# Kernel optimization log

Hardware: AMD Instinct MI355X
Metric: run time of the kernel (lower is better)

## Reference

```python
import jax, jax.numpy as jnp
import numpy as np

N = 1536       # n_nodes
D_IN = 256     # in_features
D_OUT = 64     # out_features (= n_hidden, n_heads=1, is_concat=True)
N_WAY = 16     # known_attacks_count
SLOPE = 0.2    # LeakyReLU negative slope


def setup_inputs() -> dict:
    key = jax.random.key(0)
    k1, k2, k3, k4, k5 = jax.random.split(key, 5)
    hidden_vectors = jax.random.normal(k1, (N, D_IN), dtype=jnp.float32)
    labels = jax.random.randint(k2, (N, 1), 0, N_WAY)
    zda_mask = jax.random.randint(k3, (N, 1), 0, 2).astype(bool)
    # deterministic support/query split: first half support, last half query
    query_mask = jnp.concatenate([jnp.zeros(N // 2, bool), jnp.ones(N // 2, bool)])
    W = jax.random.normal(k4, (D_OUT, D_IN), jnp.float32) * (1.0 / np.sqrt(D_IN))
    attn_w = jax.random.normal(k5, (D_OUT,), jnp.float32) * (1.0 / np.sqrt(D_OUT))
    return {"hidden_vectors": hidden_vectors, "W": W, "attn_w": attn_w,
            "labels": labels, "zda_mask": zda_mask, "query_mask": query_mask,
            "known_attacks_count": N_WAY}


def _forward(hidden_vectors, W, attn_w, labels, zda_mask, n_way):
    n = hidden_vectors.shape[0]
    dt = hidden_vectors.dtype
    # one-hot labels (scatter equivalent)
    oh = jax.nn.one_hot(labels[:, 0], n_way, dtype=dt)                 # [n, n_way]
    known = ~zda_mask[:, 0]                                            # unknown == zda
    ohm = jnp.where(known[:, None], oh, jnp.zeros((), dt))             # masked one-hot
    # collaborative kernel: semantic similarity between known pairs, else 1
    sem = ohm @ ohm.T                                                  # [n, n]
    cond = known[:, None] & known[None, :]
    kernel = jnp.where(cond, sem, jnp.ones((), dt))
    # GATv2 with shared weights, 1 head: e[i,j] = attn . lrelu(g[i] + g[j])
    g = hidden_vectors @ W.T                                           # [n, d_out]
    s = g[:, None, :] + g[None, :, :]                                  # [n, n, d_out]
    s = jnp.where(s >= 0, s, SLOPE * s)                                # LeakyReLU
    e = jnp.einsum('ijd,d->ij', s, attn_w)                             # [n, n]
    e = jnp.where(kernel == 0.0, -jnp.inf, e)                          # colaborative mask
    a = jax.nn.softmax(e, axis=1)                                      # [n, n]
    h_out = a @ g                                                      # [n, d_out] (concat, 1 head)
    # centroids over support nodes (first half)
    n_sup = n // 2
    h_sup, oh_sup = h_out[:n_sup], oh[:n_sup]
    agg = oh_sup.T @ h_sup                                             # [n_way, d_out]
    counts = oh_sup.sum(0)                                             # [n_way]
    centroids = jnp.where((counts > 0)[:, None],
                          agg / jnp.maximum(counts, 1.0)[:, None], 0.0)
    # inverse euclidean distance scores for query nodes (last half)
    hq = h_out[n_sup:]
    d2 = (jnp.sum(hq * hq, 1)[:, None] + jnp.sum(centroids * centroids, 1)[None, :]
          - 2.0 * hq @ centroids.T)
    dist = jnp.sqrt(jnp.maximum(d2, 0.0))
    scores = 1.0 / (dist + 1e-10)
    return scores, h_out, a


def reference(hidden_vectors, W, attn_w, labels, zda_mask, query_mask, known_attacks_count):
    return _forward(hidden_vectors, W, attn_w, labels, zda_mask, known_attacks_count)
```

## Files before the change

kernel.cpp:

```cpp
#include <hip/hip_runtime.h>
#include <math.h>

#define NN 1536
#define DIN 256
#define DOUT 64
#define NWAY 16
#define NSUP 768
#define IB 12
#define JBLK 256
#define SROWS 3

#define OFF_SCORES 0
#define OFF_H 12288
#define OFF_A 110592

#define WG 0
#define WQ 98304
#define WCODE 99840
#define WCENT 101376

__global__ __launch_bounds__(256) void k_g(const float* __restrict__ hid,
                                           const float* __restrict__ W,
                                           const float* __restrict__ attw,
                                           const int* __restrict__ labels,
                                           const int* __restrict__ zda,
                                           float* __restrict__ g,
                                           float* __restrict__ q,
                                           int* __restrict__ code) {
  int t = threadIdx.x;
  int r = t >> 6, d = t & 63;
  int i = blockIdx.x * 4 + r;
  const float4* hp = (const float4*)(hid + (size_t)i * DIN);
  const float4* wp = (const float4*)(W + (size_t)d * DIN);
  float4 acc = {0.f, 0.f, 0.f, 0.f};
#pragma unroll
  for (int k = 0; k < DIN / 4; k++) {
    float4 h4 = hp[k];
    float4 w4 = wp[k];
    acc.x = fmaf(h4.x, w4.x, acc.x);
    acc.y = fmaf(h4.y, w4.y, acc.y);
    acc.z = fmaf(h4.z, w4.z, acc.z);
    acc.w = fmaf(h4.w, w4.w, acc.w);
  }
  float gv = (acc.x + acc.y) + (acc.z + acc.w);
  g[(size_t)i * DOUT + d] = gv;
  float val = gv * attw[d];
#pragma unroll
  for (int off = 32; off >= 1; off >>= 1) val += __shfl_xor(val, off, 64);
  if (d == 0) q[i] = 0.6f * val;
  if (t < 4) {
    int ii = blockIdx.x * 4 + t;
    code[ii] = zda[ii] ? -1 : labels[ii];
  }
}

__global__ __launch_bounds__(256, 2) void k_e(const float* __restrict__ g,
                                              const float* __restrict__ q,
                                              const int* __restrict__ code,
                                              const float* __restrict__ attw,
                                              float* __restrict__ aout) {
  __shared__ float gis[IB * DOUT];
  __shared__ float lp[4][IB][JBLK];
  __shared__ float qi[IB];
  __shared__ int ci[IB];
  int t = threadIdx.x;
  int lane = t & 63;
  int w = t >> 6;
  int wq = __builtin_amdgcn_readfirstlane(w);
  int i0 = blockIdx.x * IB;
  int j0 = blockIdx.y * JBLK;

  if (t < IB * 16) {
    ((float4*)gis)[t] = ((const float4*)(g + (size_t)i0 * DOUT))[t];
  } else if (t < IB * 16 + IB) {
    int u = t - IB * 16;
    qi[u] = q[i0 + u];
    ci[u] = code[i0 + u];
  }
  float4 gj0[4], gj1[4], gj2[4], gj3[4];
  {
    const float4* p0 = (const float4*)(g + (size_t)(j0 + lane) * DOUT + wq * 16);
    const float4* p1 = (const float4*)(g + (size_t)(j0 + 64 + lane) * DOUT + wq * 16);
    const float4* p2 = (const float4*)(g + (size_t)(j0 + 128 + lane) * DOUT + wq * 16);
    const float4* p3 = (const float4*)(g + (size_t)(j0 + 192 + lane) * DOUT + wq * 16);
#pragma unroll
    for (int k = 0; k < 4; k++) gj0[k] = p0[k];
#pragma unroll
    for (int k = 0; k < 4; k++) gj1[k] = p1[k];
#pragma unroll
    for (int k = 0; k < 4; k++) gj2[k] = p2[k];
#pragma unroll
    for (int k = 0; k < 4; k++) gj3[k] = p3[k];
  }
  const float4* wv = (const float4*)(attw + wq * 16);
  __syncthreads();

#pragma unroll 1
  for (int u = 0; u < IB; u++) {
    const float4* gv = (const float4*)(gis + u * DOUT + wq * 16);
    float4 a0 = {0,0,0,0}, a1 = {0,0,0,0}, a2 = {0,0,0,0}, a3 = {0,0,0,0};
#pragma unroll
    for (int k = 0; k < 4; k++) {
      float4 a4 = gv[k];
      float4 w4 = wv[k];
      float4 b;
      b = gj0[k];
      a0.x = fmaf(w4.x, fabsf(a4.x + b.x), a0.x);
      a0.y = fmaf(w4.y, fabsf(a4.y + b.y), a0.y);
      a0.z = fmaf(w4.z, fabsf(a4.z + b.z), a0.z);
      a0.w = fmaf(w4.w, fabsf(a4.w + b.w), a0.w);
      b = gj1[k];
      a1.x = fmaf(w4.x, fabsf(a4.x + b.x), a1.x);
      a1.y = fmaf(w4.y, fabsf(a4.y + b.y), a1.y);
      a1.z = fmaf(w4.z, fabsf(a4.z + b.z), a1.z);
      a1.w = fmaf(w4.w, fabsf(a4.w + b.w), a1.w);
      b = gj2[k];
      a2.x = fmaf(w4.x, fabsf(a4.x + b.x), a2.x);
      a2.y = fmaf(w4.y, fabsf(a4.y + b.y), a2.y);
      a2.z = fmaf(w4.z, fabsf(a4.z + b.z), a2.z);
      a2.w = fmaf(w4.w, fabsf(a4.w + b.w), a2.w);
      b = gj3[k];
      a3.x = fmaf(w4.x, fabsf(a4.x + b.x), a3.x);
      a3.y = fmaf(w4.y, fabsf(a4.y + b.y), a3.y);
      a3.z = fmaf(w4.z, fabsf(a4.z + b.z), a3.z);
      a3.w = fmaf(w4.w, fabsf(a4.w + b.w), a3.w);
    }
    lp[w][u][lane] = (a0.x + a0.y) + (a0.z + a0.w);
    lp[w][u][lane + 64] = (a1.x + a1.y) + (a1.z + a1.w);
    lp[w][u][lane + 128] = (a2.x + a2.y) + (a2.z + a2.w);
    lp[w][u][lane + 192] = (a3.x + a3.y) + (a3.z + a3.w);
  }
  __syncthreads();

  int jg = j0 + t;
  float qj = q[jg];
  int cj = code[jg];
#pragma unroll
  for (int u = 0; u < IB; u++) {
    float s = (lp[0][u][t] + lp[1][u][t]) + (lp[2][u][t] + lp[3][u][t]);
    float e = (qi[u] + qj) + 0.4f * s;
    int cu = ci[u];
    if ((cu >= 0) && (cj >= 0) && (cu != cj)) e = -1e30f;
    aout[(size_t)(i0 + u) * NN + jg] = e;
  }
}

__global__ __launch_bounds__(512) void k_smh(float* __restrict__ a,
                                             const float* __restrict__ g,
                                             float* __restrict__ h) {
  __shared__ float buf[32 * SROWS * 68];
  __shared__ float red[16];
  float* al = buf;
  int t = threadIdx.x;
  int lane = t & 63;
  int w = t >> 6;
  int r0 = blockIdx.x * SROWS;

#pragma unroll 1
  for (int r = 0; r < SROWS; r++) {
    float* row = a + (size_t)(r0 + r) * NN;
    float v0 = row[t], v1 = row[t + 512], v2 = row[t + 1024];
    float m = fmaxf(fmaxf(v0, v1), v2);
#pragma unroll
    for (int off = 32; off >= 1; off >>= 1) m = fmaxf(m, __shfl_xor(m, off, 64));
    if (lane == 0) red[w] = m;
    __syncthreads();
    m = red[0];
#pragma unroll
    for (int k = 1; k < 8; k++) m = fmaxf(m, red[k]);
    v0 = __expf(v0 - m);
    v1 = __expf(v1 - m);
    v2 = __expf(v2 - m);
    float s = (v0 + v1) + v2;
#pragma unroll
    for (int off = 32; off >= 1; off >>= 1) s += __shfl_xor(s, off, 64);
    if (lane == 0) red[8 + w] = s;
    __syncthreads();
    s = red[8];
#pragma unroll
    for (int k = 1; k < 8; k++) s += red[8 + k];
    float inv = 1.f / s;
    v0 *= inv; v1 *= inv; v2 *= inv;
    al[r * NN + t] = v0; al[r * NN + 512 + t] = v1; al[r * NN + 1024 + t] = v2;
    row[t] = v0; row[t + 512] = v1; row[t + 1024] = v2;
    __syncthreads();
  }

  int jr = t >> 4;
  int dq = t & 15;
  float4 acc0 = {0,0,0,0}, acc1 = {0,0,0,0}, acc2 = {0,0,0,0};
#pragma unroll 4
  for (int jj = 0; jj < NN / 32; jj++) {
    int j = jj * 32 + jr;
    float4 g4 = *(const float4*)(g + (size_t)j * DOUT + dq * 4);
    float a0 = al[j], a1 = al[NN + j], a2 = al[2 * NN + j];
    acc0.x = fmaf(a0, g4.x, acc0.x); acc0.y = fmaf(a0, g4.y, acc0.y);
    acc0.z = fmaf(a0, g4.z, acc0.z); acc0.w = fmaf(a0, g4.w, acc0.w);
    acc1.x = fmaf(a1, g4.x, acc1.x); acc1.y = fmaf(a1, g4.y, acc1.y);
    acc1.z = fmaf(a1, g4.z, acc1.z); acc1.w = fmaf(a1, g4.w, acc1.w);
    acc2.x = fmaf(a2, g4.x, acc2.x); acc2.y = fmaf(a2, g4.y, acc2.y);
    acc2.z = fmaf(a2, g4.z, acc2.z); acc2.w = fmaf(a2, g4.w, acc2.w);
  }
  __syncthreads();
  *(float4*)(&buf[(jr * SROWS + 0) * 68 + dq * 4]) = acc0;
  *(float4*)(&buf[(jr * SROWS + 1) * 68 + dq * 4]) = acc1;
  *(float4*)(&buf[(jr * SROWS + 2) * 68 + dq * 4]) = acc2;
  __syncthreads();
  if (t < SROWS * DOUT) {
    int r = t >> 6, d = t & 63;
    float s = 0.f;
#pragma unroll
    for (int k = 0; k < 32; k++) s += buf[(k * SROWS + r) * 68 + d];
    h[(size_t)(r0 + r) * DOUT + d] = s;
  }
}

__global__ __launch_bounds__(1024) void k_cent(const float* __restrict__ h,
                                               const int* __restrict__ labels,
                                               float* __restrict__ cent) {
  __shared__ float part[16][64];
  __shared__ int pc[16];
  int c = blockIdx.x, t = threadIdx.x;
  int d = t & 63, rq = t >> 6;
  float acc = 0.f;
  int cnt = 0;
#pragma unroll 4
  for (int r = rq; r < NSUP; r += 16) {
    int lab = labels[r];
    if (lab == c) { acc += h[(size_t)r * DOUT + d]; cnt++; }
  }
  part[rq][d] = acc;
  if (d == 0) pc[rq] = cnt;
  __syncthreads();
  if (t < 64) {
    float num = 0.f;
    int count = 0;
#pragma unroll
    for (int k = 0; k < 16; k++) { num += part[k][t]; count += pc[k]; }
    cent[c * DOUT + t] = (count > 0) ? (num / (float)count) : 0.f;
  }
}

__global__ __launch_bounds__(256) void k_scores(const float* __restrict__ h,
                                                const float* __restrict__ cent,
                                                float* __restrict__ scores) {
  __shared__ float cl[NWAY * 65];
  __shared__ float hl[16 * 65];
  int t = threadIdx.x;
  int q0 = blockIdx.x * 16;
#pragma unroll
  for (int u = 0; u < 4; u++) {
    int f = t + u * 256;
    int row = f >> 6, k = f & 63;
    cl[row * 65 + k] = cent[f];
    hl[row * 65 + k] = h[(size_t)(NSUP + q0) * DOUT + f];
  }
  __syncthreads();
  int qr = t >> 4, c = t & 15;
  const float* hv = hl + qr * 65;
  const float* cv = cl + c * 65;
  float hh = 0.f, cc = 0.f, hc = 0.f;
#pragma unroll
  for (int k = 0; k < DOUT; k++) {
    float av = hv[k], bv = cv[k];
    hh = fmaf(av, av, hh);
    cc = fmaf(bv, bv, cc);
    hc = fmaf(av, bv, hc);
  }
  float d2 = fmaxf(hh + cc - 2.f * hc, 0.f);
  scores[q0 * NWAY + t] = 1.f / (sqrtf(d2) + 1e-10f);
}

extern "C" void kernel_launch(void* const* d_in, const int* in_sizes, int n_in,
                              void* d_out, int out_size, void* d_ws, size_t ws_size,
                              hipStream_t stream) {
  const float* hid = (const float*)d_in[0];
  const float* W = (const float*)d_in[1];
  const float* attw = (const float*)d_in[2];
  const int* labels = (const int*)d_in[3];
  const int* zda = (const int*)d_in[4];
  float* out = (float*)d_out;
  float* ws = (float*)d_ws;

  float* g = ws + WG;
  float* q = ws + WQ;
  int* code = (int*)(ws + WCODE);
  float* cent = ws + WCENT;
  float* scores = out + OFF_SCORES;
  float* h = out + OFF_H;
  float* a = out + OFF_A;

  hipLaunchKernelGGL(k_g, dim3(NN / 4), dim3(256), 0, stream, hid, W, attw, labels, zda, g, q, code);
  hipLaunchKernelGGL(k_e, dim3(NN / IB, NN / JBLK), dim3(256), 0, stream, g, q, code, attw, a);
  hipLaunchKernelGGL(k_smh, dim3(NN / SROWS), dim3(512), 0, stream, a, g, h);
  hipLaunchKernelGGL(k_cent, dim3(NWAY), dim3(1024), 0, stream, h, labels, cent);
  hipLaunchKernelGGL(k_scores, dim3(NSUP / 16), dim3(256), 0, stream, h, cent, scores);
}
```

Measured before the change: 70.10 us.

## Batch softmax reductions across six rows per 1024-thread block in k_smh

```diff
diff --git a/kernel.cpp b/kernel.cpp
--- a/kernel.cpp
+++ b/kernel.cpp
@@ -6,9 +6,9 @@
 #define DOUT 64
 #define NWAY 16
 #define NSUP 768
-#define IB 12
+#define IB 8
 #define JBLK 256
-#define SROWS 3
+#define SROWS 6
 
 #define OFF_SCORES 0
 #define OFF_H 12288
@@ -145,73 +145,107 @@
   }
 }
 
-__global__ __launch_bounds__(512) void k_smh(float* __restrict__ a,
-                                             const float* __restrict__ g,
-                                             float* __restrict__ h) {
-  __shared__ float buf[32 * SROWS * 68];
-  __shared__ float red[16];
+__global__ __launch_bounds__(1024) void k_smh(float* __restrict__ a,
+                                              const float* __restrict__ g,
+                                              float* __restrict__ h) {
+  __shared__ float buf[64 * SROWS * 68];
+  __shared__ float red[192];
   float* al = buf;
   int t = threadIdx.x;
   int lane = t & 63;
   int w = t >> 6;
   int r0 = blockIdx.x * SROWS;
-
-#pragma unroll 1
+  bool lo = (t < 512);
+
+  float v0[SROWS], v1[SROWS], m[SROWS];
+#pragma unroll
   for (int r = 0; r < SROWS; r++) {
-    float* row = a + (size_t)(r0 + r) * NN;
-    float v0 = row[t], v1 = row[t + 512], v2 = row[t + 1024];
-    float m = fmaxf(fmaxf(v0, v1), v2);
-#pragma unroll
-    for (int off = 32; off >= 1; off >>= 1) m = fmaxf(m, __shfl_xor(m, off, 64));
-    if (lane == 0) red[w] = m;
-    __syncthreads();
-    m = red[0];
-#pragma unroll
-    for (int k = 1; k < 8; k++) m = fmaxf(m, red[k]);
-    v0 = __expf(v0 - m);
-    v1 = __expf(v1 - m);
-    v2 = __expf(v2 - m);
-    float s = (v0 + v1) + v2;
-#pragma unroll
-    for (int off = 32; off >= 1; off >>= 1) s += __shfl_xor(s, off, 64);
-    if (lane == 0) red[8 + w] = s;
-    __syncthreads();
-    s = red[8];
-#pragma unroll
-    for (int k = 1; k < 8; k++) s += red[8 + k];
-    float inv = 1.f / s;
-    v0 *= inv; v1 *= inv; v2 *= inv;
-    al[r * NN + t] = v0; al[r * NN + 512 + t] = v1; al[r * NN + 1024 + t] = v2;
-    row[t] = v0; row[t + 512] = v1; row[t + 1024] = v2;
-    __syncthreads();
-  }
+    const float* row = a + (size_t)(r0 + r) * NN;
+    v0[r] = row[t];
+    v1[r] = lo ? row[1024 + t] : -3.0e38f;
+  }
+#pragma unroll
+  for (int r = 0; r < SROWS; r++) {
+    m[r] = fmaxf(v0[r], v1[r]);
+#pragma unroll
+    for (int off = 32; off >= 1; off >>= 1) m[r] = fmaxf(m[r], __shfl_xor(m[r], off, 64));
+  }
+  if (lane == 0) {
+#pragma unroll
+    for (int r = 0; r < SROWS; r++) red[w * SROWS + r] = m[r];
+  }
+  __syncthreads();
+  float s[SROWS];
+#pragma unroll
+  for (int r = 0; r < SROWS; r++) {
+    float mm = red[r];
+#pragma unroll
+    for (int k = 1; k < 16; k++) mm = fmaxf(mm, red[k * SROWS + r]);
+    v0[r] = __expf(v0[r] - mm);
+    v1[r] = lo ? __expf(v1[r] - mm) : 0.f;
+    s[r] = v0[r] + v1[r];
+#pragma unroll
+    for (int off = 32; off >= 1; off >>= 1) s[r] += __shfl_xor(s[r], off, 64);
+  }
+  if (lane == 0) {
+#pragma unroll
+    for (int r = 0; r < SROWS; r++) red[96 + w * SROWS + r] = s[r];
+  }
+  __syncthreads();
+#pragma unroll
+  for (int r = 0; r < SROWS; r++) {
+    float ss = red[96 + r];
+#pragma unroll
+    for (int k = 1; k < 16; k++) ss += red[96 + k * SROWS + r];
+    float inv = 1.f / ss;
+    float a0 = v0[r] * inv;
+    al[r * NN + t] = a0;
+    a[(size_t)(r0 + r) * NN + t] = a0;
+    if (lo) {
+      float a1 = v1[r] * inv;
+      al[r * NN + 1024 + t] = a1;
+      a[(size_t)(r0 + r) * NN + 1024 + t] = a1;
+    }
+  }
+  __syncthreads();
 
   int jr = t >> 4;
   int dq = t & 15;
   float4 acc0 = {0,0,0,0}, acc1 = {0,0,0,0}, acc2 = {0,0,0,0};
+  float4 acc3 = {0,0,0,0}, acc4 = {0,0,0,0}, acc5 = {0,0,0,0};
 #pragma unroll 4
-  for (int jj = 0; jj < NN / 32; jj++) {
-    int j = jj * 32 + jr;
+  for (int jj = 0; jj < NN / 64; jj++) {
+    int j = jj * 64 + jr;
     float4 g4 = *(const float4*)(g + (size_t)j * DOUT + dq * 4);
     float a0 = al[j], a1 = al[NN + j], a2 = al[2 * NN + j];
+    float a3 = al[3 * NN + j], a4 = al[4 * NN + j], a5 = al[5 * NN + j];
     acc0.x = fmaf(a0, g4.x, acc0.x); acc0.y = fmaf(a0, g4.y, acc0.y);
     acc0.z = fmaf(a0, g4.z, acc0.z); acc0.w = fmaf(a0, g4.w, acc0.w);
     acc1.x = fmaf(a1, g4.x, acc1.x); acc1.y = fmaf(a1, g4.y, acc1.y);
     acc1.z = fmaf(a1, g4.z, acc1.z); acc1.w = fmaf(a1, g4.w, acc1.w);
     acc2.x = fmaf(a2, g4.x, acc2.x); acc2.y = fmaf(a2, g4.y, acc2.y);
     acc2.z = fmaf(a2, g4.z, acc2.z); acc2.w = fmaf(a2, g4.w, acc2.w);
+    acc3.x = fmaf(a3, g4.x, acc3.x); acc3.y = fmaf(a3, g4.y, acc3.y);
+    acc3.z = fmaf(a3, g4.z, acc3.z); acc3.w = fmaf(a3, g4.w, acc3.w);
+    acc4.x = fmaf(a4, g4.x, acc4.x); acc4.y = fmaf(a4, g4.y, acc4.y);
+    acc4.z = fmaf(a4, g4.z, acc4.z); acc4.w = fmaf(a4, g4.w, acc4.w);
+    acc5.x = fmaf(a5, g4.x, acc5.x); acc5.y = fmaf(a5, g4.y, acc5.y);
+    acc5.z = fmaf(a5, g4.z, acc5.z); acc5.w = fmaf(a5, g4.w, acc5.w);
   }
   __syncthreads();
   *(float4*)(&buf[(jr * SROWS + 0) * 68 + dq * 4]) = acc0;
   *(float4*)(&buf[(jr * SROWS + 1) * 68 + dq * 4]) = acc1;
   *(float4*)(&buf[(jr * SROWS + 2) * 68 + dq * 4]) = acc2;
+  *(float4*)(&buf[(jr * SROWS + 3) * 68 + dq * 4]) = acc3;
+  *(float4*)(&buf[(jr * SROWS + 4) * 68 + dq * 4]) = acc4;
+  *(float4*)(&buf[(jr * SROWS + 5) * 68 + dq * 4]) = acc5;
   __syncthreads();
   if (t < SROWS * DOUT) {
     int r = t >> 6, d = t & 63;
-    float s = 0.f;
-#pragma unroll
-    for (int k = 0; k < 32; k++) s += buf[(k * SROWS + r) * 68 + d];
-    h[(size_t)(r0 + r) * DOUT + d] = s;
+    float ssum = 0.f;
+#pragma unroll
+    for (int k = 0; k < 64; k++) ssum += buf[(k * SROWS + r) * 68 + d];
+    h[(size_t)(r0 + r) * DOUT + d] = ssum;
   }
 }
 
@@ -292,7 +326,7 @@
 
   hipLaunchKernelGGL(k_g, dim3(NN / 4), dim3(256), 0, stream, hid, W, attw, labels, zda, g, q, code);
   hipLaunchKernelGGL(k_e, dim3(NN / IB, NN / JBLK), dim3(256), 0, stream, g, q, code, attw, a);
-  hipLaunchKernelGGL(k_smh, dim3(NN / SROWS), dim3(512), 0, stream, a, g, h);
+  hipLaunchKernelGGL(k_smh, dim3(NN / SROWS), dim3(1024), 0, stream, a, g, h);
   hipLaunchKernelGGL(k_cent, dim3(NWAY), dim3(1024), 0, stream, h, labels, cent);
   hipLaunchKernelGGL(k_scores, dim3(NSUP / 16), dim3(256), 0, stream, h, cent, scores);
 }
```

New measurement: 73.47 us. +4.8%, slower.
